# Performance work log

Measured on AMD Instinct MI355X. Metric: run time of the kernel, lower is better.

The kernel has to match this reference:

```python
import jax, jax.numpy as jnp
import numpy as np

N = 100000      # nodes
E = 320000      # edges
G = 2048        # graphs
NODE_F, EDGE_F, HID, EDGE_DIM, L = 48, 6, 256, 128, 8


def setup_inputs() -> dict:
    key = jax.random.key(0)
    ks = jax.random.split(key, 16)
    s = 0.05
    return dict(
        x=jax.random.normal(ks[0], (N, NODE_F), jnp.float32),
        edge_attr=jax.random.normal(ks[1], (E, EDGE_F), jnp.float32),
        node_w=jax.random.normal(ks[2], (NODE_F, HID), jnp.float32) * s,
        node_b=jnp.zeros((HID,), jnp.float32),
        edge_w=jax.random.normal(ks[3], (EDGE_F, EDGE_DIM), jnp.float32) * s,
        edge_b=jnp.zeros((EDGE_DIM,), jnp.float32),
        conv_edge_w=jax.random.normal(ks[4], (L, EDGE_DIM, HID), jnp.float32) * s,
        conv_edge_b=jnp.zeros((L, HID), jnp.float32),
        mlp_w1=jax.random.normal(ks[5], (L, HID, HID), jnp.float32) * s,
        mlp_b1=jnp.zeros((L, HID), jnp.float32),
        mlp_w2=jax.random.normal(ks[6], (L, HID, HID), jnp.float32) * s,
        mlp_b2=jnp.zeros((L, HID), jnp.float32),
        eps=jnp.zeros((L,), jnp.float32),  # GINE trainable eps, init 0
        bn_gamma=jnp.ones((L, HID), jnp.float32),
        bn_beta=jnp.zeros((L, HID), jnp.float32),
        att_w1=jax.random.normal(ks[7], (HID, HID // 2), jnp.float32) * s,
        att_b1=jnp.zeros((HID // 2,), jnp.float32),
        att_w2=jax.random.normal(ks[8], (HID // 2, 1), jnp.float32) * s,
        att_b2=jnp.zeros((1,), jnp.float32),
        edge_index=jax.random.randint(ks[9], (2, E), 0, N),
        batch=jnp.sort(jax.random.randint(ks[10], (N,), 0, G)),
        num_graphs=G,
    )


def reference(x, edge_attr, node_w, node_b, edge_w, edge_b, conv_edge_w, conv_edge_b,
              mlp_w1, mlp_b1, mlp_w2, mlp_b2, eps, bn_gamma, bn_beta,
              att_w1, att_b1, att_w2, att_b2, edge_index, batch, num_graphs):
    seg_sum = lambda v, ids, n: jax.ops.segment_sum(v, ids, num_segments=n)
    n_nodes = x.shape[0]
    src, dst = edge_index[0], edge_index[1]  # x_j gathered from src, aggregated at dst

    h = x @ node_w + node_b                      # node embedding [N, HID]
    e = edge_attr @ edge_w + edge_b              # edge embedding [E, EDGE_DIM]
    cnt = jnp.maximum(seg_sum(jnp.ones((n_nodes,), h.dtype), batch, num_graphs), 1.0)

    for i in range(conv_edge_w.shape[0]):
        # GINEConv: msg = ReLU(x_j + Lin(edge_emb)); add-aggregate; MLP((1+eps)x + agg)
        ee = e @ conv_edge_w[i] + conv_edge_b[i]             # [E, HID]
        msg = jax.nn.relu(h[src] + ee)
        agg = seg_sum(msg, dst, n_nodes)
        z = (1.0 + eps[i]) * h + agg
        z = jax.nn.relu(z @ mlp_w1[i] + mlp_b1[i]) @ mlp_w2[i] + mlp_b2[i]
        # BatchNorm1d (batch statistics, biased var, eps=1e-5)
        mu = z.mean(0)
        var = z.var(0)
        z = bn_gamma[i] * (z - mu) * jax.lax.rsqrt(var + 1e-5) + bn_beta[i]
        # PairNorm (per-graph center, then normalize by sqrt(eps + mean sq norm))
        gmean = seg_sum(z, batch, num_graphs) / cnt[:, None]
        z = z - gmean[batch]
        msq = seg_sum(jnp.sum(z * z, axis=-1), batch, num_graphs) / cnt
        z = z * jax.lax.rsqrt(1e-5 + msq)[batch][:, None]
        h = jax.nn.relu(z)

    # pooling: mean + max + attention (exp-score softmax per graph)
    mean_pool = seg_sum(h, batch, num_graphs) / cnt[:, None]
    max_pool = jax.ops.segment_max(h, batch, num_segments=num_graphs)
    max_pool = jnp.where(jnp.isfinite(max_pool), max_pool, 0.0)
    scores = jnp.tanh(h @ att_w1 + att_b1) @ att_w2 + att_b2   # [N, 1]
    w = jnp.exp(scores)
    w = w / (seg_sum(w, batch, num_graphs)[batch] + 1e-8)
    att_pool = seg_sum(h * w, batch, num_graphs)
    return jnp.concatenate([mean_pool, max_pool, att_pool], axis=-1)  # [G, 768]
```

## Files before the change

### kernel.cpp

```cpp
#include <hip/hip_runtime.h>
#include <cstdint>
#include <cstddef>

#define NN 100000
#define EE 320000
#define GG 2048
#define LL 8

#define O_Z    0ull
#define O_ZB   25600000ull
#define O_HB   38400000ull
#define O_S1   51200000ull
#define O_S2   (O_S1 + 524288ull)
#define O_ABUF (O_S2 + 524288ull)
#define O_BBUF (O_ABUF + 256ull)
#define O_CNTI (O_BBUF + 256ull)
#define O_CNTF (O_CNTI + 2048ull)
#define O_SCOR (O_CNTF + 2048ull)
#define O_WEFF (O_SCOR + 100000ull)
#define O_BEFF (O_WEFF + 12288ull)
#define O_DEG  (O_BEFF + 2048ull)
#define O_STRT (O_DEG + 100000ull)
#define O_BSUM (O_STRT + 100000ull)
#define O_CSR  (O_BSUM + 512ull)
#define O_W1P  (O_CSR + 1280000ull)
#define O_W2P  (O_W1P + 262144ull)
#define O_ATP  (O_W2P + 262144ull)
#define O_GST  (O_ATP + 16384ull)

typedef short s16x8 __attribute__((ext_vector_type(8)));
typedef float f32x4 __attribute__((ext_vector_type(4)));

__device__ inline float b2f(unsigned int lo16) {
  union { float f; unsigned int u; } x; x.u = lo16 << 16; return x.f;
}
__device__ inline unsigned short f2b(float f) {
  union { float f; unsigned int u; } x; x.f = f;
  unsigned int r = x.u + 0x7FFFu + ((x.u >> 16) & 1u);
  return (unsigned short)(r >> 16);
}

__global__ __launch_bounds__(256) void k_zero(float* __restrict__ p, int n) {
  int i = blockIdx.x * 256 + threadIdx.x;
  int stride = gridDim.x * 256;
  for (; i < n; i += stride) p[i] = 0.0f;
}

__global__ __launch_bounds__(256) void k_count(const int* __restrict__ batch, int* __restrict__ cnti, int n) {
  int i = blockIdx.x * 256 + threadIdx.x;
  if (i < n) atomicAdd(&cnti[batch[i]], 1);
}

__global__ __launch_bounds__(256) void k_gscan(const int* __restrict__ cnti, int* __restrict__ gstart,
                                               float* __restrict__ cntf) {
  __shared__ int part[256];
  int t = threadIdx.x;
  int base = t * 8;
  int loc[8];
  int s = 0;
#pragma unroll
  for (int i = 0; i < 8; ++i) { loc[i] = s; s += cnti[base + i]; }
  part[t] = s;
  __syncthreads();
  for (int off = 1; off < 256; off <<= 1) {
    int u = (t >= off) ? part[t - off] : 0;
    __syncthreads();
    part[t] += u;
    __syncthreads();
  }
  int p = (t > 0) ? part[t - 1] : 0;
#pragma unroll
  for (int i = 0; i < 8; ++i) {
    gstart[base + i] = p + loc[i];
    float v = (float)cnti[base + i];
    cntf[base + i] = v > 1.0f ? v : 1.0f;
  }
}

__global__ __launch_bounds__(256) void k_deg(const int* __restrict__ edst, int* __restrict__ deg, int ne) {
  int e = blockIdx.x * 256 + threadIdx.x;
  if (e < ne) atomicAdd(&deg[edst[e]], 1);
}

__global__ __launch_bounds__(256) void k_scan_part(const int* __restrict__ deg, int* __restrict__ start,
                                                   int* __restrict__ bsum, int n) {
  __shared__ int s[256];
  int i = blockIdx.x * 256 + threadIdx.x;
  int t = threadIdx.x;
  int v = (i < n) ? deg[i] : 0;
  s[t] = v;
  __syncthreads();
  for (int off = 1; off < 256; off <<= 1) {
    int u = (t >= off) ? s[t - off] : 0;
    __syncthreads();
    s[t] += u;
    __syncthreads();
  }
  if (i < n) start[i] = s[t] - v;
  if (t == 255) bsum[blockIdx.x] = s[255];
}

__global__ __launch_bounds__(512) void k_scan_top(int* __restrict__ bsum, int nb) {
  __shared__ int s[512];
  int t = threadIdx.x;
  int v = (t < nb) ? bsum[t] : 0;
  s[t] = v;
  __syncthreads();
  for (int off = 1; off < 512; off <<= 1) {
    int u = (t >= off) ? s[t - off] : 0;
    __syncthreads();
    s[t] += u;
    __syncthreads();
  }
  if (t < nb) bsum[t] = s[t] - v;
}

__global__ __launch_bounds__(256) void k_scan_add(int* __restrict__ start, const int* __restrict__ bsum,
                                                  int* __restrict__ cursor, int n) {
  int i = blockIdx.x * 256 + threadIdx.x;
  if (i < n) {
    int v = start[i] + bsum[blockIdx.x];
    start[i] = v;
    cursor[i] = v;
  }
}

__global__ __launch_bounds__(256) void k_fill(const float* __restrict__ ea, const int* __restrict__ esrc,
                                              const int* __restrict__ edst, int* __restrict__ cursor,
                                              uint4* __restrict__ csr, int ne) {
  int e = blockIdx.x * 256 + threadIdx.x;
  if (e >= ne) return;
  int d = edst[e];
  int slot = atomicAdd(&cursor[d], 1);
  const float* ap = ea + (size_t)e * 6;
  uint4 v;
  v.x = (unsigned int)f2b(ap[0]) | ((unsigned int)f2b(ap[1]) << 16);
  v.y = (unsigned int)f2b(ap[2]) | ((unsigned int)f2b(ap[3]) << 16);
  v.z = (unsigned int)f2b(ap[4]) | ((unsigned int)f2b(ap[5]) << 16);
  v.w = (unsigned int)esrc[e];
  csr[slot] = v;
}

__global__ __launch_bounds__(256) void k_wfuse(const float* __restrict__ edge_w, const float* __restrict__ edge_b,
                                               const float* __restrict__ conv_w, const float* __restrict__ conv_b,
                                               float* __restrict__ wef, float* __restrict__ bef) {
  __shared__ float ew[6 * 128 + 128];
  int i = blockIdx.x;
  int c = threadIdx.x;
  for (int idx = c; idx < 896; idx += 256)
    ew[idx] = idx < 768 ? edge_w[idx] : edge_b[idx - 768];
  __syncthreads();
  float acc[7] = {0.f, 0.f, 0.f, 0.f, 0.f, 0.f, 0.f};
  const float* cw = conv_w + (size_t)i * 32768 + c;
  for (int j = 0; j < 128; ++j) {
    float w = cw[(size_t)j * 256];
#pragma unroll
    for (int k = 0; k < 6; ++k) acc[k] = fmaf(ew[k * 128 + j], w, acc[k]);
    acc[6] = fmaf(ew[768 + j], w, acc[6]);
  }
#pragma unroll
  for (int k = 0; k < 6; ++k) wef[(size_t)i * 1536 + k * 256 + c] = acc[k];
  bef[(size_t)i * 256 + c] = acc[6] + conv_b[(size_t)i * 256 + c];
}

__global__ __launch_bounds__(256) void k_pack_all(const float* __restrict__ mw1, const float* __restrict__ mw2,
                                                  const float* __restrict__ aw1,
                                                  unsigned short* __restrict__ w1p,
                                                  unsigned short* __restrict__ w2p,
                                                  unsigned short* __restrict__ atp) {
  int id = blockIdx.x * 256 + threadIdx.x;
  int cbu = id >> 12;
  if (cbu >= 33) return;
  int lid = id & 4095;
  int l = lid & 63;
  int ct = (lid >> 6) & 7;
  int ks = (lid >> 9) & 7;
  const float* B;
  unsigned short* Bp;
  int ldb, cb;
  if (cbu < 32) {
    int m = cbu >> 1;
    cb = cbu & 1;
    ldb = 256;
    if (m < 8) { B = mw1 + (size_t)m * 65536; Bp = w1p + (size_t)m * 65536; }
    else       { B = mw2 + (size_t)(m - 8) * 65536; Bp = w2p + (size_t)(m - 8) * 65536; }
  } else {
    B = aw1; Bp = atp; ldb = 128; cb = 0;
  }
  int n = cb * 128 + ct * 16 + (l & 15);
  int k0 = ks * 32 + (l >> 4) * 8;
  unsigned short* dst = Bp + (((size_t)cb << 12) | (size_t)lid) * 8;
#pragma unroll
  for (int j = 0; j < 8; ++j) dst[j] = f2b(B[(size_t)(k0 + j) * ldb + n]);
}

__global__ __launch_bounds__(256) void k_node_embed(const float* __restrict__ x, const float* __restrict__ w,
                                                    const float* __restrict__ b, unsigned short* __restrict__ hb,
                                                    int n) {
  __shared__ float xs[16 * 48];
  int tid = threadIdx.x;
  int row0 = blockIdx.x * 16;
  for (int idx = tid; idx < 16 * 48; idx += 256) {
    int r = idx / 48, c = idx - r * 48;
    int gr = row0 + r; if (gr >= n) gr = n - 1;
    xs[idx] = x[(size_t)gr * 48 + c];
  }
  __syncthreads();
  float acc[16];
#pragma unroll
  for (int r = 0; r < 16; ++r) acc[r] = 0.0f;
  for (int k = 0; k < 48; ++k) {
    float wv = w[k * 256 + tid];
#pragma unroll
    for (int r = 0; r < 16; ++r) acc[r] = fmaf(xs[r * 48 + k], wv, acc[r]);
  }
  float bb = b[tid];
#pragma unroll
  for (int r = 0; r < 16; ++r) {
    int gr = row0 + r;
    if (gr < n) hb[(size_t)gr * 256 + tid] = f2b(acc[r] + bb);
  }
}

__global__ __launch_bounds__(256) void k_edge_csr(const uint4* __restrict__ csr,
                                                  const int* __restrict__ startv, const int* __restrict__ degv,
                                                  const float* __restrict__ wef, const float* __restrict__ bef,
                                                  const unsigned short* __restrict__ hb,
                                                  unsigned short* __restrict__ zb,
                                                  const float* __restrict__ eps, int layer, int n) {
  int lane = threadIdx.x & 63;
  int wv = threadIdx.x >> 6;
  int v0 = (blockIdx.x * 4 + wv) * 4;
  if (v0 >= n) return;
  int c0 = lane * 4;
  float4 w0 = *(const float4*)(wef + 0 * 256 + c0);
  float4 w1 = *(const float4*)(wef + 1 * 256 + c0);
  float4 w2 = *(const float4*)(wef + 2 * 256 + c0);
  float4 w3 = *(const float4*)(wef + 3 * 256 + c0);
  float4 w4 = *(const float4*)(wef + 4 * 256 + c0);
  float4 w5 = *(const float4*)(wef + 5 * 256 + c0);
  float4 bf = *(const float4*)(bef + c0);
  float s = 1.0f + eps[layer];

  int dg[4], pp[4];
  float4 acc[4];
#pragma unroll
  for (int k = 0; k < 4; ++k) {
    int v = v0 + k;
    dg[k] = degv[v];
    int st = startv[v];
    pp[k] = st < (EE - 1) ? st : (EE - 1);
    uint2 hu = *(const uint2*)(hb + (size_t)v * 256 + c0);
    acc[k].x = s * b2f(hu.x & 0xFFFFu);
    acc[k].y = s * b2f(hu.x >> 16);
    acc[k].z = s * b2f(hu.y & 0xFFFFu);
    acc[k].w = s * b2f(hu.y >> 16);
  }
  int mx = dg[0] > dg[1] ? dg[0] : dg[1];
  int mx2 = dg[2] > dg[3] ? dg[2] : dg[3];
  if (mx2 > mx) mx = mx2;

  for (int t = 0; t < mx; ++t) {
    uint4 e[4];
#pragma unroll
    for (int k = 0; k < 4; ++k) e[k] = csr[pp[k]];
    uint2 g[4];
#pragma unroll
    for (int k = 0; k < 4; ++k) g[k] = *(const uint2*)(hb + (size_t)(int)e[k].w * 256 + c0);
#pragma unroll
    for (int k = 0; k < 4; ++k) {
      if (t < dg[k]) {
        float a0 = b2f(e[k].x & 0xFFFFu), a1 = b2f(e[k].x >> 16), a2 = b2f(e[k].y & 0xFFFFu);
        float a3 = b2f(e[k].y >> 16), a4 = b2f(e[k].z & 0xFFFFu), a5 = b2f(e[k].z >> 16);
        float mxv = fmaf(a0, w0.x, fmaf(a1, w1.x, fmaf(a2, w2.x, fmaf(a3, w3.x, fmaf(a4, w4.x, fmaf(a5, w5.x, b2f(g[k].x & 0xFFFFu) + bf.x))))));
        float myv = fmaf(a0, w0.y, fmaf(a1, w1.y, fmaf(a2, w2.y, fmaf(a3, w3.y, fmaf(a4, w4.y, fmaf(a5, w5.y, b2f(g[k].x >> 16) + bf.y))))));
        float mzv = fmaf(a0, w0.z, fmaf(a1, w1.z, fmaf(a2, w2.z, fmaf(a3, w3.z, fmaf(a4, w4.z, fmaf(a5, w5.z, b2f(g[k].y & 0xFFFFu) + bf.z))))));
        float mwv = fmaf(a0, w0.w, fmaf(a1, w1.w, fmaf(a2, w2.w, fmaf(a3, w3.w, fmaf(a4, w4.w, fmaf(a5, w5.w, b2f(g[k].y >> 16) + bf.w))))));
        acc[k].x += mxv > 0.f ? mxv : 0.f;
        acc[k].y += myv > 0.f ? myv : 0.f;
        acc[k].z += mzv > 0.f ? mzv : 0.f;
        acc[k].w += mwv > 0.f ? mwv : 0.f;
      }
      pp[k] += (t < dg[k] - 1) ? 1 : 0;
    }
  }
#pragma unroll
  for (int k = 0; k < 4; ++k) {
    uint2 o;
    o.x = (unsigned int)f2b(acc[k].x) | ((unsigned int)f2b(acc[k].y) << 16);
    o.y = (unsigned int)f2b(acc[k].z) | ((unsigned int)f2b(acc[k].w) << 16);
    *(uint2*)(zb + (size_t)(v0 + k) * 256 + c0) = o;
  }
}

__global__ __launch_bounds__(256, 4) void k_mlp(const unsigned short* __restrict__ A,
                                                const unsigned short* __restrict__ W1p,
                                                const float* __restrict__ b1,
                                                const unsigned short* __restrict__ W2p,
                                                const float* __restrict__ b2,
                                                float* __restrict__ Z, int M) {
  __shared__ __align__(16) unsigned char smem[33024];
  unsigned short* t1s = (unsigned short*)smem;
  float* zc = (float*)smem;
  int l = threadIdx.x & 63;
  int w = threadIdx.x >> 6;
  int mloc = l & 15, q = l >> 4;
  int rowg = (w & 1) * 32;
  int colh = (w >> 1) * 128;
  int row0 = blockIdx.x * 64;

  const unsigned short* ap[2];
#pragma unroll
  for (int rt = 0; rt < 2; ++rt) {
    int r = row0 + rowg + rt * 16 + mloc;
    if (r > M - 1) r = M - 1;
    ap[rt] = A + (size_t)r * 256 + q * 8;
  }
  f32x4 acc[2][8];
#pragma unroll
  for (int rt = 0; rt < 2; ++rt)
#pragma unroll
    for (int ct = 0; ct < 8; ++ct) acc[rt][ct] = (f32x4){0.f, 0.f, 0.f, 0.f};

  const unsigned short* w1base = W1p + ((size_t)(colh >> 7)) * 32768 + (size_t)l * 8;
#pragma unroll
  for (int ks = 0; ks < 8; ++ks) {
    s16x8 a0 = *(const s16x8*)(ap[0] + ks * 32);
    s16x8 a1 = *(const s16x8*)(ap[1] + ks * 32);
#pragma unroll
    for (int ct = 0; ct < 8; ++ct) {
      s16x8 b = *(const s16x8*)(w1base + ks * 4096 + ct * 512);
      acc[0][ct] = __builtin_amdgcn_mfma_f32_16x16x32_bf16(a0, b, acc[0][ct], 0, 0, 0);
      acc[1][ct] = __builtin_amdgcn_mfma_f32_16x16x32_bf16(a1, b, acc[1][ct], 0, 0, 0);
    }
  }
#pragma unroll
  for (int ct = 0; ct < 8; ++ct) {
    int col = colh + ct * 16 + mloc;
    float bv = b1[col];
    int cc = col >> 3, pos = col & 7;
#pragma unroll
    for (int rt = 0; rt < 2; ++rt)
#pragma unroll
      for (int r = 0; r < 4; ++r) {
        int row = rowg + rt * 16 + q * 4 + r;
        float v = acc[rt][ct][r] + bv;
        v = v > 0.f ? v : 0.f;
        t1s[row * 256 + ((cc ^ (row & 31)) << 3) + pos] = f2b(v);
      }
  }
  __syncthreads();
#pragma unroll
  for (int rt = 0; rt < 2; ++rt)
#pragma unroll
    for (int ct = 0; ct < 8; ++ct) acc[rt][ct] = (f32x4){0.f, 0.f, 0.f, 0.f};
  const unsigned short* w2base = W2p + ((size_t)(colh >> 7)) * 32768 + (size_t)l * 8;
#pragma unroll
  for (int ks = 0; ks < 8; ++ks) {
    s16x8 a[2];
#pragma unroll
    for (int rt = 0; rt < 2; ++rt) {
      int row = rowg + rt * 16 + mloc;
      int cc = (q + ks * 4) ^ (row & 31);
      a[rt] = *(const s16x8*)(t1s + row * 256 + (cc << 3));
    }
#pragma unroll
    for (int ct = 0; ct < 8; ++ct) {
      s16x8 b = *(const s16x8*)(w2base + ks * 4096 + ct * 512);
      acc[0][ct] = __builtin_amdgcn_mfma_f32_16x16x32_bf16(a[0], b, acc[0][ct], 0, 0, 0);
      acc[1][ct] = __builtin_amdgcn_mfma_f32_16x16x32_bf16(a[1], b, acc[1][ct], 0, 0, 0);
    }
  }
  float bv2[8];
#pragma unroll
  for (int ct = 0; ct < 8; ++ct) bv2[ct] = b2[colh + ct * 16 + mloc];

#pragma unroll
  for (int half = 0; half < 2; ++half) {
    __syncthreads();
    if ((w & 1) == half) {
#pragma unroll
      for (int ct = 0; ct < 8; ++ct) {
        int col = colh + ct * 16 + mloc;
#pragma unroll
        for (int rt = 0; rt < 2; ++rt)
#pragma unroll
          for (int r = 0; r < 4; ++r) {
            int row = rt * 16 + q * 4 + r;
            zc[row * 258 + col] = acc[rt][ct][r] + bv2[ct];
          }
      }
    }
    __syncthreads();
    int baserow = row0 + half * 32;
#pragma unroll
    for (int it = 0; it < 8; ++it) {
      int row = it * 4 + w;
      int grow = baserow + row;
      float4 vv = *(const float4*)(zc + row * 258 + l * 4);
      if (grow < M) *(float4*)(Z + (size_t)grow * 256 + l * 4) = vv;
    }
  }
}

__global__ __launch_bounds__(256) void k_att(const unsigned short* __restrict__ A,
                                             const unsigned short* __restrict__ Bp,
                                             const float* __restrict__ b1,
                                             const float* __restrict__ w2,
                                             const float* __restrict__ b2,
                                             float* __restrict__ scores, int M) {
  int l = threadIdx.x & 63;
  int w = threadIdx.x >> 6;
  int mloc = l & 15, q = l >> 4;
  int row0 = blockIdx.x * 128 + w * 32;

  int r0 = row0 + mloc;      if (r0 > M - 1) r0 = M - 1;
  int r1 = row0 + 16 + mloc; if (r1 > M - 1) r1 = M - 1;
  const unsigned short* ap0 = A + (size_t)r0 * 256 + q * 8;
  const unsigned short* ap1 = A + (size_t)r1 * 256 + q * 8;
  const unsigned short* bp = Bp + (size_t)l * 8;

  f32x4 acc[2][8];
#pragma unroll
  for (int rt = 0; rt < 2; ++rt)
#pragma unroll
    for (int ct = 0; ct < 8; ++ct) acc[rt][ct] = (f32x4){0.f, 0.f, 0.f, 0.f};
#pragma unroll
  for (int ks = 0; ks < 8; ++ks) {
    s16x8 a0 = *(const s16x8*)(ap0 + ks * 32);
    s16x8 a1 = *(const s16x8*)(ap1 + ks * 32);
#pragma unroll
    for (int ct = 0; ct < 8; ++ct) {
      s16x8 b = *(const s16x8*)(bp + ks * 4096 + ct * 512);
      acc[0][ct] = __builtin_amdgcn_mfma_f32_16x16x32_bf16(a0, b, acc[0][ct], 0, 0, 0);
      acc[1][ct] = __builtin_amdgcn_mfma_f32_16x16x32_bf16(a1, b, acc[1][ct], 0, 0, 0);
    }
  }
  float bv[8], wv[8];
#pragma unroll
  for (int ct = 0; ct < 8; ++ct) {
    bv[ct] = b1[ct * 16 + mloc];
    wv[ct] = w2[ct * 16 + mloc];
  }
  float b2v = b2[0];
#pragma unroll
  for (int rt = 0; rt < 2; ++rt)
#pragma unroll
    for (int r = 0; r < 4; ++r) {
      float p = 0.0f;
#pragma unroll
      for (int ct = 0; ct < 8; ++ct) p = fmaf(tanhf(acc[rt][ct][r] + bv[ct]), wv[ct], p);
      p += __shfl_xor(p, 1, 64);
      p += __shfl_xor(p, 2, 64);
      p += __shfl_xor(p, 4, 64);
      p += __shfl_xor(p, 8, 64);
      int row = row0 + rt * 16 + q * 4 + r;
      if (mloc == 0 && row < M) scores[row] = p + b2v;
    }
}

__global__ __launch_bounds__(256) void k_stats(const float* __restrict__ z, const int* __restrict__ gstart,
                                               const int* __restrict__ cnti,
                                               float* __restrict__ S1, float* __restrict__ S2) {
  int g = blockIdx.x, c = threadIdx.x;
  int r0 = gstart[g], r1 = r0 + cnti[g];
  float s1 = 0.0f, s2 = 0.0f;
  for (int r = r0; r < r1; ++r) {
    float v = z[(size_t)r * 256 + c];
    s1 += v;
    s2 = fmaf(v, v, s2);
  }
  S1[(size_t)g * 256 + c] = s1;
  S2[(size_t)g * 256 + c] = s2;
}

__global__ __launch_bounds__(256) void k_bn_fin(const float* __restrict__ S1, const float* __restrict__ S2,
                                                const float* __restrict__ gamma, const float* __restrict__ beta,
                                                float* __restrict__ abuf, float* __restrict__ bbuf, int n) {
  __shared__ float r1[256], r2[256];
  int c = blockIdx.x;
  int t = threadIdx.x;
  float s1 = 0.0f, s2 = 0.0f;
  for (int g = t; g < GG; g += 256) {
    s1 += S1[(size_t)g * 256 + c];
    s2 += S2[(size_t)g * 256 + c];
  }
  r1[t] = s1; r2[t] = s2;
  __syncthreads();
  for (int off = 128; off; off >>= 1) {
    if (t < off) { r1[t] += r1[t + off]; r2[t] += r2[t + off]; }
    __syncthreads();
  }
  if (t == 0) {
    float inv = 1.0f / (float)n;
    float mu = r1[0] * inv;
    float var = r2[0] * inv - mu * mu;
    float rstd = rsqrtf(var + 1e-5f);
    float a = gamma[c] * rstd;
    abuf[c] = a;
    bbuf[c] = beta[c] - mu * a;
  }
}

template <int LAST>
__global__ __launch_bounds__(256) void k_apply(float* __restrict__ z, const float* __restrict__ abuf,
                                               const float* __restrict__ bbuf, const int* __restrict__ gstart,
                                               const int* __restrict__ cnti, const float* __restrict__ cntf,
                                               const float* __restrict__ S1, const float* __restrict__ S2,
                                               unsigned short* __restrict__ hb) {
  __shared__ float rT[256], rM[256];
  int g = blockIdx.x, c = threadIdx.x;
  float a = abuf[c], b = bbuf[c];
  float s1 = S1[(size_t)g * 256 + c];
  float s2 = S2[(size_t)g * 256 + c];
  float nr = (float)cnti[g];
  float ic = 1.0f / cntf[g];
  float mean = (a * s1 + nr * b) * ic;
  float term = fmaf(a * a, s2, fmaf(2.0f * a * b, s1, nr * b * b));
  rT[c] = term;
  rM[c] = mean * mean;
  __syncthreads();
  for (int off = 128; off; off >>= 1) {
    if (c < off) { rT[c] += rT[c + off]; rM[c] += rM[c + off]; }
    __syncthreads();
  }
  float cr = nr > 0.0f ? 1.0f : 0.0f;
  float rinv = rsqrtf(1e-5f + rT[0] * ic - cr * rM[0]);
  int r0 = gstart[g], r1 = r0 + cnti[g];
  for (int r = r0; r < r1; ++r) {
    float v = (fmaf(a, z[(size_t)r * 256 + c], b) - mean) * rinv;
    v = v > 0.0f ? v : 0.0f;
    hb[(size_t)r * 256 + c] = f2b(v);
    if (LAST) z[(size_t)r * 256 + c] = v;
  }
}

__global__ __launch_bounds__(256) void k_poolout(const float* __restrict__ h, const float* __restrict__ scores,
                                                 const int* __restrict__ gstart, const int* __restrict__ cnti,
                                                 const float* __restrict__ cntf, float* __restrict__ out) {
  int g = blockIdx.x, c = threadIdx.x;
  int r0 = gstart[g], r1 = r0 + cnti[g];
  float ma = 0.0f, aa = 0.0f, mx = 0.0f, wa = 0.0f;
  for (int r = r0; r < r1; ++r) {
    float wgt = __expf(scores[r]);
    float hv = h[(size_t)r * 256 + c];
    ma += hv;
    aa = fmaf(hv, wgt, aa);
    mx = fmaxf(mx, hv);
    wa += wgt;
  }
  out[(size_t)g * 768 + c] = ma / cntf[g];
  out[(size_t)g * 768 + 256 + c] = mx;
  out[(size_t)g * 768 + 512 + c] = aa / (wa + 1e-8f);
}

extern "C" void kernel_launch(void* const* d_in, const int* in_sizes, int n_in,
                              void* d_out, int out_size, void* d_ws, size_t ws_size,
                              hipStream_t stream) {
  const float* x         = (const float*)d_in[0];
  const float* edge_attr = (const float*)d_in[1];
  const float* node_w    = (const float*)d_in[2];
  const float* node_b    = (const float*)d_in[3];
  const float* edge_w    = (const float*)d_in[4];
  const float* edge_b    = (const float*)d_in[5];
  const float* conv_w    = (const float*)d_in[6];
  const float* conv_b    = (const float*)d_in[7];
  const float* mlp_w1    = (const float*)d_in[8];
  const float* mlp_b1    = (const float*)d_in[9];
  const float* mlp_w2    = (const float*)d_in[10];
  const float* mlp_b2    = (const float*)d_in[11];
  const float* eps       = (const float*)d_in[12];
  const float* bn_gamma  = (const float*)d_in[13];
  const float* bn_beta   = (const float*)d_in[14];
  const float* att_w1    = (const float*)d_in[15];
  const float* att_b1    = (const float*)d_in[16];
  const float* att_w2    = (const float*)d_in[17];
  const float* att_b2    = (const float*)d_in[18];
  const int*   eidx      = (const int*)d_in[19];
  const int*   batch     = (const int*)d_in[20];
  float* out = (float*)d_out;
  float* ws  = (float*)d_ws;

  float*          zbuf = ws + O_Z;
  unsigned short* zb   = (unsigned short*)(ws + O_ZB);
  unsigned short* hb   = (unsigned short*)(ws + O_HB);
  float* S1    = ws + O_S1;
  float* S2    = ws + O_S2;
  float* abuf  = ws + O_ABUF;
  float* bbuf  = ws + O_BBUF;
  int*   cnti  = (int*)(ws + O_CNTI);
  float* cntf  = ws + O_CNTF;
  float* scor  = ws + O_SCOR;
  int*   curs  = (int*)(ws + O_SCOR);
  float* weff  = ws + O_WEFF;
  float* beff  = ws + O_BEFF;
  int*   deg   = (int*)(ws + O_DEG);
  int*   strt  = (int*)(ws + O_STRT);
  int*   bsum  = (int*)(ws + O_BSUM);
  uint4* csr   = (uint4*)(ws + O_CSR);
  unsigned short* w1p = (unsigned short*)(ws + O_W1P);
  unsigned short* w2p = (unsigned short*)(ws + O_W2P);
  unsigned short* atp = (unsigned short*)(ws + O_ATP);
  int*   gst   = (int*)(ws + O_GST);
  const int* esrc = eidx;
  const int* edst = eidx + EE;

  k_zero<<<8, 256, 0, stream>>>((float*)cnti, GG);
  k_count<<<(NN + 255) / 256, 256, 0, stream>>>(batch, cnti, NN);
  k_gscan<<<1, 256, 0, stream>>>(cnti, gst, cntf);

  k_wfuse<<<LL, 256, 0, stream>>>(edge_w, edge_b, conv_w, conv_b, weff, beff);
  k_node_embed<<<(NN + 15) / 16, 256, 0, stream>>>(x, node_w, node_b, hb, NN);
  k_pack_all<<<528, 256, 0, stream>>>(mlp_w1, mlp_w2, att_w1, w1p, w2p, atp);

  const int nscan = (NN + 255) / 256;
  k_zero<<<256, 256, 0, stream>>>((float*)deg, NN);
  k_deg<<<(EE + 255) / 256, 256, 0, stream>>>(edst, deg, EE);
  k_scan_part<<<nscan, 256, 0, stream>>>(deg, strt, bsum, NN);
  k_scan_top<<<1, 512, 0, stream>>>(bsum, nscan);
  k_scan_add<<<nscan, 256, 0, stream>>>(strt, bsum, curs, NN);
  k_fill<<<(EE + 255) / 256, 256, 0, stream>>>(edge_attr, esrc, edst, curs, csr, EE);

  const int mtiles64  = (NN + 63) / 64;
  const int mtiles128 = (NN + 127) / 128;

  for (int i = 0; i < LL; ++i) {
    k_edge_csr<<<NN / 16, 256, 0, stream>>>(csr, strt, deg, weff + (size_t)i * 1536,
                                            beff + (size_t)i * 256, hb, zb, eps, i, NN);
    k_mlp<<<mtiles64, 256, 0, stream>>>(zb, w1p + (size_t)i * 65536, mlp_b1 + (size_t)i * 256,
                                        w2p + (size_t)i * 65536, mlp_b2 + (size_t)i * 256, zbuf, NN);
    k_stats<<<GG, 256, 0, stream>>>(zbuf, gst, cnti, S1, S2);
    k_bn_fin<<<256, 256, 0, stream>>>(S1, S2, bn_gamma + (size_t)i * 256, bn_beta + (size_t)i * 256,
                                      abuf, bbuf, NN);
    if (i == LL - 1)
      k_apply<1><<<GG, 256, 0, stream>>>(zbuf, abuf, bbuf, gst, cnti, cntf, S1, S2, hb);
    else
      k_apply<0><<<GG, 256, 0, stream>>>(zbuf, abuf, bbuf, gst, cnti, cntf, S1, S2, hb);
  }

  k_att<<<mtiles128, 256, 0, stream>>>(hb, atp, att_b1, att_w2, att_b2, scor, NN);
  k_poolout<<<GG, 256, 0, stream>>>(zbuf, scor, gst, cnti, cntf, out);
}
```

Measured before the change: 1.810 ms.

## Fuse per-graph stats into MLP epilogue and use MFMA for node embedding

Per-graph column sums and sums of squares are now computed in the k_mlp epilogue from the shared-memory tile and added to S1/S2 with atomics. This removes the separate k_stats pass that re-read the full fp32 Z buffer every layer. k_apply zeroes S1/S2 after reading them so they are ready for the next layer. The node embedding is rewritten as a bf16 MFMA kernel that splits x into hi and lo bf16 parts to keep accuracy, with a new weight-packing kernel. The cost is added atomic traffic and a slightly different embedding precision.

```diff
diff --git a/kernel.cpp b/kernel.cpp
--- a/kernel.cpp
+++ b/kernel.cpp
@@ -27,6 +27,7 @@
 #define O_W2P  (O_W1P + 262144ull)
 #define O_ATP  (O_W2P + 262144ull)
 #define O_GST  (O_ATP + 16384ull)
+#define O_NWP  (O_GST + 2048ull)
 
 typedef short s16x8 __attribute__((ext_vector_type(8)));
 typedef float f32x4 __attribute__((ext_vector_type(4)));
@@ -38,6 +39,11 @@
   union { float f; unsigned int u; } x; x.f = f;
   unsigned int r = x.u + 0x7FFFu + ((x.u >> 16) & 1u);
   return (unsigned short)(r >> 16);
+}
+__device__ inline unsigned short f2b_lo(float v) {
+  unsigned short h = f2b(v);
+  float hf = b2f((unsigned int)h);
+  return f2b(v - hf);
 }
 
 __global__ __launch_bounds__(256) void k_zero(float* __restrict__ p, int n) {
@@ -194,31 +200,81 @@
   for (int j = 0; j < 8; ++j) dst[j] = f2b(B[(size_t)(k0 + j) * ldb + n]);
 }
 
-__global__ __launch_bounds__(256) void k_node_embed(const float* __restrict__ x, const float* __restrict__ w,
-                                                    const float* __restrict__ b, unsigned short* __restrict__ hb,
-                                                    int n) {
-  __shared__ float xs[16 * 48];
-  int tid = threadIdx.x;
-  int row0 = blockIdx.x * 16;
-  for (int idx = tid; idx < 16 * 48; idx += 256) {
-    int r = idx / 48, c = idx - r * 48;
-    int gr = row0 + r; if (gr >= n) gr = n - 1;
-    xs[idx] = x[(size_t)gr * 48 + c];
-  }
-  __syncthreads();
-  float acc[16];
-#pragma unroll
-  for (int r = 0; r < 16; ++r) acc[r] = 0.0f;
-  for (int k = 0; k < 48; ++k) {
-    float wv = w[k * 256 + tid];
-#pragma unroll
-    for (int r = 0; r < 16; ++r) acc[r] = fmaf(xs[r * 48 + k], wv, acc[r]);
-  }
-  float bb = b[tid];
-#pragma unroll
-  for (int r = 0; r < 16; ++r) {
-    int gr = row0 + r;
-    if (gr < n) hb[(size_t)gr * 256 + tid] = f2b(acc[r] + bb);
+__global__ __launch_bounds__(256) void k_pack_node(const float* __restrict__ w,
+                                                   unsigned short* __restrict__ Wp) {
+  int id = blockIdx.x * 256 + threadIdx.x;
+  if (id >= 3072) return;
+  int l = id & 63;
+  int t = id >> 6;
+  int ct = t & 7;
+  int u = t >> 3;
+  int ks = u % 3;
+  int cb = u / 3;
+  int n = cb * 128 + ct * 16 + (l & 15);
+  unsigned short* dst = Wp + (size_t)id * 8;
+#pragma unroll
+  for (int j = 0; j < 8; ++j) {
+    int kk = ks * 32 + ((l >> 4) << 3) + j;
+    int ksrc = kk < 48 ? kk : kk - 48;
+    dst[j] = f2b(w[(size_t)ksrc * 256 + n]);
+  }
+}
+
+__global__ __launch_bounds__(256) void k_embed_mfma(const float* __restrict__ x,
+                                                    const unsigned short* __restrict__ Wp,
+                                                    const float* __restrict__ b,
+                                                    unsigned short* __restrict__ hb, int M) {
+  int l = threadIdx.x & 63;
+  int w = threadIdx.x >> 6;
+  int mloc = l & 15, q = l >> 4;
+  int row0 = blockIdx.x * 64 + (w & 1) * 32;
+  int colh = (w >> 1) * 128;
+
+  f32x4 acc[2][8];
+#pragma unroll
+  for (int rt = 0; rt < 2; ++rt)
+#pragma unroll
+    for (int ct = 0; ct < 8; ++ct) acc[rt][ct] = (f32x4){0.f, 0.f, 0.f, 0.f};
+
+  union { s16x8 v; unsigned short u[8]; } a[2][3];
+#pragma unroll
+  for (int rt = 0; rt < 2; ++rt) {
+    int r = row0 + rt * 16 + mloc;
+    if (r > M - 1) r = M - 1;
+    const float* xr = x + (size_t)r * 48;
+    const float* p0 = xr + q * 8;
+    const float* p1 = xr + (q < 2 ? 32 + q * 8 : (q - 2) * 8);
+    const float* p2 = xr + 16 + q * 8;
+#pragma unroll
+    for (int j = 0; j < 8; ++j) {
+      a[rt][0].u[j] = f2b(p0[j]);
+      a[rt][1].u[j] = (q < 2) ? f2b(p1[j]) : f2b_lo(p1[j]);
+      a[rt][2].u[j] = f2b_lo(p2[j]);
+    }
+  }
+
+  const unsigned short* bp = Wp + (size_t)(colh >> 7) * 12288 + (size_t)l * 8;
+#pragma unroll
+  for (int ks = 0; ks < 3; ++ks) {
+#pragma unroll
+    for (int ct = 0; ct < 8; ++ct) {
+      s16x8 bb = *(const s16x8*)(bp + ks * 4096 + ct * 512);
+      acc[0][ct] = __builtin_amdgcn_mfma_f32_16x16x32_bf16(a[0][ks].v, bb, acc[0][ct], 0, 0, 0);
+      acc[1][ct] = __builtin_amdgcn_mfma_f32_16x16x32_bf16(a[1][ks].v, bb, acc[1][ct], 0, 0, 0);
+    }
+  }
+
+#pragma unroll
+  for (int ct = 0; ct < 8; ++ct) {
+    int col = colh + ct * 16 + mloc;
+    float bv = b[col];
+#pragma unroll
+    for (int rt = 0; rt < 2; ++rt)
+#pragma unroll
+      for (int r = 0; r < 4; ++r) {
+        int row = row0 + rt * 16 + q * 4 + r;
+        if (row < M) hb[(size_t)row * 256 + col] = f2b(acc[rt][ct][r] + bv);
+      }
   }
 }
 
@@ -298,7 +354,9 @@
                                                 const float* __restrict__ b1,
                                                 const unsigned short* __restrict__ W2p,
                                                 const float* __restrict__ b2,
-                                                float* __restrict__ Z, int M) {
+                                                float* __restrict__ Z,
+                                                const int* __restrict__ batchv,
+                                                float* __restrict__ S1, float* __restrict__ S2, int M) {
   __shared__ __align__(16) unsigned char smem[33024];
   unsigned short* t1s = (unsigned short*)smem;
   float* zc = (float*)smem;
@@ -399,6 +457,27 @@
       int grow = baserow + row;
       float4 vv = *(const float4*)(zc + row * 258 + l * 4);
       if (grow < M) *(float4*)(Z + (size_t)grow * 256 + l * 4) = vv;
+    }
+    {
+      int c = threadIdx.x;
+      int rend = (M - baserow) < 32 ? (M - baserow) : 32;
+      if (rend > 0) {
+        float s1 = 0.f, s2 = 0.f;
+        int gcur = batchv[baserow];
+        for (int row = 0; row < rend; ++row) {
+          int g = batchv[baserow + row];
+          if (g != gcur) {
+            atomicAdd(&S1[(size_t)gcur * 256 + c], s1);
+            atomicAdd(&S2[(size_t)gcur * 256 + c], s2);
+            s1 = 0.f; s2 = 0.f; gcur = g;
+          }
+          float v = zc[row * 258 + c];
+          s1 += v;
+          s2 = fmaf(v, v, s2);
+        }
+        atomicAdd(&S1[(size_t)gcur * 256 + c], s1);
+        atomicAdd(&S2[(size_t)gcur * 256 + c], s2);
+      }
     }
   }
 }
@@ -459,21 +538,6 @@
     }
 }
 
-__global__ __launch_bounds__(256) void k_stats(const float* __restrict__ z, const int* __restrict__ gstart,
-                                               const int* __restrict__ cnti,
-                                               float* __restrict__ S1, float* __restrict__ S2) {
-  int g = blockIdx.x, c = threadIdx.x;
-  int r0 = gstart[g], r1 = r0 + cnti[g];
-  float s1 = 0.0f, s2 = 0.0f;
-  for (int r = r0; r < r1; ++r) {
-    float v = z[(size_t)r * 256 + c];
-    s1 += v;
-    s2 = fmaf(v, v, s2);
-  }
-  S1[(size_t)g * 256 + c] = s1;
-  S2[(size_t)g * 256 + c] = s2;
-}
-
 __global__ __launch_bounds__(256) void k_bn_fin(const float* __restrict__ S1, const float* __restrict__ S2,
                                                 const float* __restrict__ gamma, const float* __restrict__ beta,
                                                 float* __restrict__ abuf, float* __restrict__ bbuf, int n) {
@@ -506,13 +570,16 @@
 __global__ __launch_bounds__(256) void k_apply(float* __restrict__ z, const float* __restrict__ abuf,
                                                const float* __restrict__ bbuf, const int* __restrict__ gstart,
                                                const int* __restrict__ cnti, const float* __restrict__ cntf,
-                                               const float* __restrict__ S1, const float* __restrict__ S2,
+                                               float* __restrict__ S1, float* __restrict__ S2,
                                                unsigned short* __restrict__ hb) {
   __shared__ float rT[256], rM[256];
   int g = blockIdx.x, c = threadIdx.x;
   float a = abuf[c], b = bbuf[c];
-  float s1 = S1[(size_t)g * 256 + c];
-  float s2 = S2[(size_t)g * 256 + c];
+  size_t idx = (size_t)g * 256 + c;
+  float s1 = S1[idx];
+  float s2 = S2[idx];
+  S1[idx] = 0.0f;
+  S2[idx] = 0.0f;
   float nr = (float)cnti[g];
   float ic = 1.0f / cntf[g];
   float mean = (a * s1 + nr * b) * ic;
@@ -602,6 +669,7 @@
   unsigned short* w2p = (unsigned short*)(ws + O_W2P);
   unsigned short* atp = (unsigned short*)(ws + O_ATP);
   int*   gst   = (int*)(ws + O_GST);
+  unsigned short* nwp = (unsigned short*)(ws + O_NWP);
   const int* esrc = eidx;
   const int* edst = eidx + EE;
 
@@ -610,8 +678,11 @@
   k_gscan<<<1, 256, 0, stream>>>(cnti, gst, cntf);
 
   k_wfuse<<<LL, 256, 0, stream>>>(edge_w, edge_b, conv_w, conv_b, weff, beff);
-  k_node_embed<<<(NN + 15) / 16, 256, 0, stream>>>(x, node_w, node_b, hb, NN);
   k_pack_all<<<528, 256, 0, stream>>>(mlp_w1, mlp_w2, att_w1, w1p, w2p, atp);
+  k_pack_node<<<12, 256, 0, stream>>>(node_w, nwp);
+  k_embed_mfma<<<(NN + 63) / 64, 256, 0, stream>>>(x, nwp, node_b, hb, NN);
+
+  k_zero<<<1024, 256, 0, stream>>>(S1, 2 * 524288);
 
   const int nscan = (NN + 255) / 256;
   k_zero<<<256, 256, 0, stream>>>((float*)deg, NN);
@@ -628,8 +699,8 @@
     k_edge_csr<<<NN / 16, 256, 0, stream>>>(csr, strt, deg, weff + (size_t)i * 1536,
                                             beff + (size_t)i * 256, hb, zb, eps, i, NN);
     k_mlp<<<mtiles64, 256, 0, stream>>>(zb, w1p + (size_t)i * 65536, mlp_b1 + (size_t)i * 256,
-                                        w2p + (size_t)i * 65536, mlp_b2 + (size_t)i * 256, zbuf, NN);
-    k_stats<<<GG, 256, 0, stream>>>(zbuf, gst, cnti, S1, S2);
+                                        w2p + (size_t)i * 65536, mlp_b2 + (size_t)i * 256, zbuf,
+                                        batch, S1, S2, NN);
     k_bn_fin<<<256, 256, 0, stream>>>(S1, S2, bn_gamma + (size_t)i * 256, bn_beta + (size_t)i * 256,
                                       abuf, bbuf, NN);
     if (i == LL - 1)
```

Result: faster. 1.705 ms (-5.8%).
